# Kernel tuning notes

Hardware: AMD Instinct MI355X
Metric: run time of the kernel (lower is better)

Reference implementation:

```python
import jax, jax.numpy as jnp
import numpy as np

D_MODEL, D_STATE, D_CONV, EXPAND = 1024, 16, 4, 2
D_INNER = EXPAND * D_MODEL            # 2048
DT_RANK = (D_MODEL + 15) // 16        # 64 (mamba 'auto')
B, L = 2, 2048
EPS = 1e-5


def setup_inputs() -> dict:
    key = jax.random.key(0)
    ks = jax.random.split(key, 12)
    s = lambda k, shape, sc=0.02: jax.random.normal(k, shape, dtype=jnp.float32) * sc
    return {
        "x": jax.random.normal(ks[0], (B, L, D_MODEL), dtype=jnp.float32),
        "ln_w": jnp.ones((D_MODEL,), jnp.float32),
        "ln_b": jnp.zeros((D_MODEL,), jnp.float32),
        "W_in": s(ks[1], (2 * D_INNER, D_MODEL)),
        "conv_w": s(ks[2], (D_INNER, D_CONV), 0.2),
        "conv_b": jnp.zeros((D_INNER,), jnp.float32),
        "W_xproj": s(ks[3], (DT_RANK + 2 * D_STATE, D_INNER)),
        "W_dt": s(ks[4], (D_INNER, DT_RANK), 0.1),
        "b_dt": jax.random.uniform(ks[5], (D_INNER,), jnp.float32, -4.0, -2.0),  # softplus(b)~dt_min
        "A_log": jnp.log(jnp.broadcast_to(jnp.arange(1, D_STATE + 1, dtype=jnp.float32), (D_INNER, D_STATE))),
        "D": jnp.ones((D_INNER,), jnp.float32),
        "W_out": s(ks[6], (D_MODEL, D_INNER)),
    }


def _mamba_forward(x, ln_w, ln_b, W_in, conv_w, conv_b, W_xproj, W_dt, b_dt, A_log, D, W_out):
    # Pre-norm LayerNorm
    mu = jnp.mean(x, axis=-1, keepdims=True)
    var = jnp.mean(jnp.square(x - mu), axis=-1, keepdims=True)
    xn = (x - mu) * jax.lax.rsqrt(var + EPS) * ln_w + ln_b

    # in_proj -> [B, L, 2*d_inner]; split into x-branch and gate z
    xz = jnp.einsum("bld,ed->ble", xn, W_in)
    u, z = jnp.split(xz, 2, axis=-1)

    # causal depthwise conv1d over L, kernel width D_CONV
    u_pad = jnp.pad(u, ((0, 0), (D_CONV - 1, 0), (0, 0)))
    uc = conv_b[None, None, :]
    for k in range(D_CONV):
        uc = uc + u_pad[:, k:k + L, :] * conv_w[:, k]
    u = jax.nn.silu(uc)  # [B, L, d_inner]

    # input-dependent dt, B, C
    dbl = jnp.einsum("bld,ed->ble", u, W_xproj)
    dt_r = dbl[..., :DT_RANK]
    Bm = dbl[..., DT_RANK:DT_RANK + D_STATE]          # [B, L, n]
    Cm = dbl[..., DT_RANK + D_STATE:]                 # [B, L, n]
    dt = jax.nn.softplus(jnp.einsum("blr,dr->bld", dt_r, W_dt) + b_dt)  # [B, L, d]

    A = -jnp.exp(A_log)  # [d, n]

    # selective scan over L; carry h: [B, d, n]
    def step(h, inp):
        dt_t, B_t, C_t, u_t = inp  # [B,d], [B,n], [B,n], [B,d]
        dA = jnp.exp(dt_t[:, :, None] * A[None])                 # [B, d, n]
        h = dA * h + (dt_t * u_t)[:, :, None] * B_t[:, None, :]  # [B, d, n]
        y_t = jnp.einsum("bdn,bn->bd", h, C_t)
        return h, y_t

    xs = (jnp.moveaxis(dt, 1, 0), jnp.moveaxis(Bm, 1, 0),
          jnp.moveaxis(Cm, 1, 0), jnp.moveaxis(u, 1, 0))
    h0 = jnp.zeros((x.shape[0], D_INNER, D_STATE), x.dtype)
    _, ys = jax.lax.scan(step, h0, xs)
    y = jnp.moveaxis(ys, 0, 1) + u * D  # [B, L, d_inner]

    y = y * jax.nn.silu(z)
    out = jnp.einsum("bld,ed->ble", y, W_out)
    return x + out


def reference(x, ln_w, ln_b, W_in, conv_w, conv_b, W_xproj, W_dt, b_dt, A_log, D, W_out):
    return _mamba_forward(x, ln_w, ln_b, W_in, conv_w, conv_b, W_xproj, W_dt, b_dt, A_log, D, W_out)
```

## Files before the change

### kernel.cpp

```cpp
#include <hip/hip_runtime.h>
#include <hip/hip_bf16.h>
#include <stdint.h>

typedef __hip_bfloat16 bf16;
typedef __attribute__((ext_vector_type(8))) short short8;
typedef __attribute__((ext_vector_type(4))) short short4v;
typedef __attribute__((ext_vector_type(4))) float floatx4;

#define D_MODEL 1024
#define D_STATE 16
#define D_INNER 2048
#define DT_RANK 64
#define BB 2
#define LL 2048
#define BL (BB * LL)
#define XZ_LD (2 * D_INNER)
#define DBL_LD (DT_RANK + 2 * D_STATE)
#define NCH 64
#define TCH (LL / NCH)

__device__ __forceinline__ bf16 f2b(float f) { return __float2bfloat16(f); }

__device__ __forceinline__ float fsig(float v)  { return __fdividef(1.f, 1.f + __expf(-v)); }
__device__ __forceinline__ float fsoftp(float v){ return fmaxf(v, 0.f) + __logf(1.f + __expf(-fabsf(v))); }

__device__ __forceinline__ void gload16(const void* g, void* l) {
    __builtin_amdgcn_global_load_lds(
        (const __attribute__((address_space(1))) uint32_t*)(uintptr_t)g,
        (__attribute__((address_space(3))) uint32_t*)(uintptr_t)l,
        16, 0, 0);
}

#define S0 (4096 * 1024)
#define S1 (128 * 2048)
#define S2 (2048 * 64)
#define S3 (1024 * 2048)
#define S4 (BL * DBL_LD)
#define WCVT_TOT (S0 + S1 + S2 + S3 + S4)
#define WCVT4 (WCVT_TOT / 4)

__device__ __forceinline__ void cvt4(const float* __restrict__ src,
                                     bf16* __restrict__ dst, int qi) {
    const floatx4 v = *(const floatx4*)(src + (size_t)qi * 4);
    short4v o;
#pragma unroll
    for (int j = 0; j < 4; ++j) {
        bf16 h = f2b(v[j]);
        unsigned short us;
        __builtin_memcpy(&us, &h, 2);
        o[j] = (short)us;
    }
    *(short4v*)(dst + (size_t)qi * 4) = o;
}

__global__ __launch_bounds__(256) void prep_kernel(
    const float* __restrict__ x, const float* __restrict__ w,
    const float* __restrict__ b, bf16* __restrict__ xnb,
    const float* __restrict__ Win, const float* __restrict__ Wx,
    const float* __restrict__ Wdt, const float* __restrict__ Wout,
    bf16* __restrict__ win_bf, bf16* __restrict__ wx_bf,
    bf16* __restrict__ wdt_bf, bf16* __restrict__ wout_bf,
    float* __restrict__ dbl)
{
    __shared__ float s1[256], s2[256];
    const int tid = threadIdx.x;
    if (blockIdx.x < BL) {
        const int row = blockIdx.x;
        const float* xr = x + (size_t)row * D_MODEL;
        float v[4], sum = 0.f, sq = 0.f;
#pragma unroll
        for (int i = 0; i < 4; ++i) {
            v[i] = xr[tid + 256 * i];
            sum += v[i];
            sq  += v[i] * v[i];
        }
        s1[tid] = sum; s2[tid] = sq;
        __syncthreads();
        for (int s = 128; s > 0; s >>= 1) {
            if (tid < s) { s1[tid] += s1[tid + s]; s2[tid] += s2[tid + s]; }
            __syncthreads();
        }
        const float mu  = s1[0] * (1.f / D_MODEL);
        const float var = s2[0] * (1.f / D_MODEL) - mu * mu;
        const float rs  = rsqrtf(var + 1e-5f);
#pragma unroll
        for (int i = 0; i < 4; ++i) {
            const int c = tid + 256 * i;
            xnb[(size_t)row * D_MODEL + c] = f2b((v[i] - mu) * rs * w[c] + b[c]);
        }
    } else {
        int id = (blockIdx.x - BL) * 256 + tid;
        if (id < S0 / 4) { cvt4(Win, win_bf, id); return; }
        id -= S0 / 4;
        if (id < S1 / 4) {
            if (id < (96 * 2048) / 4) cvt4(Wx, wx_bf, id);
            else *(short4v*)(wx_bf + (size_t)id * 4) = (short4v){0, 0, 0, 0};
            return;
        }
        id -= S1 / 4;
        if (id < S2 / 4) { cvt4(Wdt, wdt_bf, id); return; }
        id -= S2 / 4;
        if (id < S3 / 4) { cvt4(Wout, wout_bf, id); return; }
        id -= S3 / 4;
        *(floatx4*)(dbl + (size_t)id * 4) = (floatx4){0.f, 0.f, 0.f, 0.f};
    }
}

#define GTM 128
#define GTN 128
#define GTK 32

template <int EPI>
__global__ __launch_bounds__(256) void gemm_t(
    const bf16* __restrict__ A, int lda,
    const bf16* __restrict__ B, int ldb,
    float* __restrict__ C, int ldc,
    int N, int K,
    const float* __restrict__ bias,
    bf16* __restrict__ C2)
{
    __shared__ short As[GTM * GTK];
    __shared__ short Bs[GTN * GTK];
    const int tid  = threadIdx.x;
    const int lane = tid & 63;
    const int wave = tid >> 6;
    const int wm = (wave & 1) * 64;
    const int wn = (wave >> 1) * 64;
    const int bm = blockIdx.y * GTM;
    const int bn = blockIdx.x * GTN;
    const int kbase = blockIdx.z * K;

    floatx4 acc[4][4];
#pragma unroll
    for (int i = 0; i < 4; ++i)
#pragma unroll
        for (int j = 0; j < 4; ++j) acc[i][j] = (floatx4){0.f, 0.f, 0.f, 0.f};

    const int srow = wave * 16 + (lane >> 2);
    const int scol = (lane & 3) * 8;
    const int fm = lane & 15;
    const int q  = lane >> 4;

    for (int k0 = 0; k0 < K; k0 += GTK) {
#pragma unroll
        for (int r = 0; r < 2; ++r) {
            const int m = r * 64 + srow;
            gload16(A + (size_t)(bm + m) * lda + kbase + k0 + scol,
                    As + m * GTK + scol);
            gload16(B + (size_t)(bn + m) * ldb + kbase + k0 + scol,
                    Bs + m * GTK + scol);
        }
        __syncthreads();

        short8 af[4], bfr[4];
#pragma unroll
        for (int i = 0; i < 4; ++i)
            af[i] = *(short8*)&As[(wm + i * 16 + fm) * GTK + q * 8];
#pragma unroll
        for (int j = 0; j < 4; ++j)
            bfr[j] = *(short8*)&Bs[(wn + j * 16 + fm) * GTK + q * 8];
#pragma unroll
        for (int i = 0; i < 4; ++i)
#pragma unroll
            for (int j = 0; j < 4; ++j)
                acc[i][j] = __builtin_amdgcn_mfma_f32_16x16x32_bf16(
                    af[i], bfr[j], acc[i][j], 0, 0, 0);
        __syncthreads();
    }

    const int col = lane & 15;
    const int rq  = (lane >> 4) * 4;
#pragma unroll
    for (int i = 0; i < 4; ++i) {
#pragma unroll
        for (int j = 0; j < 4; ++j) {
#pragma unroll
            for (int r = 0; r < 4; ++r) {
                const int gm = bm + wm + i * 16 + rq + r;
                const int gn = bn + wn + j * 16 + col;
                if (gn >= N) continue;
                float v = acc[i][j][r];
                if constexpr (EPI == 3) {
                    atomicAdd(&C[(size_t)gm * ldc + gn], v);
                } else if constexpr (EPI == 4) {
                    if (gn < D_INNER) C[(size_t)gm * ldc + gn] = v;
                    else C2[(size_t)gm * (size_t)D_INNER + (gn - D_INNER)] = f2b(v);
                } else {
                    C2[(size_t)gm * ldc + gn] = f2b(fsoftp(v + bias[gn]));
                }
            }
        }
    }
}

#define PNT (D_MODEL / 64)

__global__ __launch_bounds__(512, 2) void gemm256_uz(
    const bf16* __restrict__ A,
    const bf16* __restrict__ B,
    float* __restrict__ U,
    bf16* __restrict__ Z)
{
    __shared__ __attribute__((aligned(16))) short lds[65536];
    const int t    = threadIdx.x;
    const int lane = t & 63;
    const int wid  = t >> 6;
    const int wm   = wid >> 2;
    const int wn   = wid & 3;
    const int fm   = lane & 15;
    const int q    = lane >> 4;

    const int lin = (int)blockIdx.x;
    const int nid = (lin & 7) * 32 + (lin >> 3);
    const int bm  = (nid >> 4) * 256;
    const int bn  = (nid & 15) * 256;

    const int sg   = (((t & 7) ^ ((t >> 3) & 7)) << 3);
    const int ldst = t * 8;
    const short* Agp = (const short*)A + (size_t)(bm + (t >> 3)) * D_MODEL + sg;
    const short* Bgp = (const short*)B + (size_t)(bn + (t >> 3)) * D_MODEL + sg;

#define STG(g, lb) do { \
        gload16((g),                           &lds[(lb) + ldst]);        \
        gload16((g) + (size_t)64 * D_MODEL,    &lds[(lb) + 4096 + ldst]); \
    } while (0)

    const int ss0 = ((q ^ (fm & 7)) << 3);
    const int ss1 = (((4 + q) ^ (fm & 7)) << 3);
    const int aro = fm * 64;
    const int bro = ((wn & 1) * 64 + fm) * 64;

    floatx4 acc[8][4];
#pragma unroll
    for (int i = 0; i < 8; ++i)
#pragma unroll
        for (int j = 0; j < 4; ++j) acc[i][j] = (floatx4){0.f, 0.f, 0.f, 0.f};

    STG(Agp, 0);
    STG(Agp + (size_t)128 * D_MODEL, 8192);
    STG(Bgp, 32768);
    STG(Bgp + (size_t)128 * D_MODEL, 32768 + 8192);

    for (int kt = 0; kt < PNT; ++kt) {
        __syncthreads();
        const int d  = kt & 1;
        const short* Ab = &lds[d * 16384 + wm * 8192];
        const short* Bb = &lds[32768 + d * 16384 + (wn >> 1) * 8192];
        const int kn = (kt + 1) * 64;
        const int nb = (d ^ 1) * 16384;

        short8 bfr[4][2];
#pragma unroll
        for (int cf = 0; cf < 4; ++cf) {
            bfr[cf][0] = *(const short8*)(Bb + bro + cf * 1024 + ss0);
            bfr[cf][1] = *(const short8*)(Bb + bro + cf * 1024 + ss1);
        }

#pragma unroll
        for (int qd = 0; qd < 4; ++qd) {
            short8 af[2][2];
#pragma unroll
            for (int i = 0; i < 2; ++i) {
                af[i][0] = *(const short8*)(Ab + (qd * 2 + i) * 1024 + aro + ss0);
                af[i][1] = *(const short8*)(Ab + (qd * 2 + i) * 1024 + aro + ss1);
            }
            if (qd == 0 && kt < PNT - 1) {
                STG(Agp + kn,                        nb);
                STG(Agp + (size_t)128 * D_MODEL + kn, nb + 8192);
            }
            if (qd == 1 && kt < PNT - 1) {
                STG(Bgp + kn,                        32768 + nb);
                STG(Bgp + (size_t)128 * D_MODEL + kn, 32768 + nb + 8192);
            }
            __builtin_amdgcn_s_barrier();
            __builtin_amdgcn_s_setprio(1);
#pragma unroll
            for (int i = 0; i < 2; ++i)
#pragma unroll
                for (int cf = 0; cf < 4; ++cf) {
                    acc[qd * 2 + i][cf] = __builtin_amdgcn_mfma_f32_16x16x32_bf16(
                        af[i][0], bfr[cf][0], acc[qd * 2 + i][cf], 0, 0, 0);
                    acc[qd * 2 + i][cf] = __builtin_amdgcn_mfma_f32_16x16x32_bf16(
                        af[i][1], bfr[cf][1], acc[qd * 2 + i][cf], 0, 0, 0);
                }
            __builtin_amdgcn_s_setprio(0);
            if (qd < 3) __builtin_amdgcn_s_barrier();
        }
    }
#undef STG

    const int gm0 = bm + wm * 128 + q * 4;
    const int gn0 = bn + wn * 64 + fm;
    if (bn < D_INNER) {
#pragma unroll
        for (int rf = 0; rf < 8; ++rf)
#pragma unroll
            for (int cf = 0; cf < 4; ++cf)
#pragma unroll
                for (int r = 0; r < 4; ++r)
                    U[(size_t)(gm0 + rf * 16 + r) * D_INNER + gn0 + cf * 16] =
                        acc[rf][cf][r];
    } else {
#pragma unroll
        for (int rf = 0; rf < 8; ++rf)
#pragma unroll
            for (int cf = 0; cf < 4; ++cf)
#pragma unroll
                for (int r = 0; r < 4; ++r)
                    Z[(size_t)(gm0 + rf * 16 + r) * D_INNER + gn0 + cf * 16 - D_INNER] =
                        f2b(acc[rf][cf][r]);
    }
}

#define ONT (D_INNER / 64)

__global__ __launch_bounds__(512, 2) void gemm_out8(
    const bf16* __restrict__ A,
    const bf16* __restrict__ B,
    const float* __restrict__ resid,
    float* __restrict__ C)
{
    __shared__ __attribute__((aligned(16))) short lds[32768];
    const int t    = threadIdx.x;
    const int lane = t & 63;
    const int wid  = t >> 6;
    const int wm   = wid >> 2;
    const int wn   = wid & 3;
    const int fm   = lane & 15;
    const int q    = lane >> 4;

    const int lin = (int)blockIdx.x;
    const int nid = (lin & 7) * 32 + (lin >> 3);
    const int bm  = (nid >> 3) * 128;
    const int bn  = (nid & 7) * 128;

    const int sg   = (((t & 7) ^ ((t >> 3) & 7)) << 3);
    const int ldst = t * 8;
    const short* Agp = (const short*)A + (size_t)(bm + (t >> 3)) * D_INNER + sg;
    const short* Bgp = (const short*)B + (size_t)(bn + (t >> 3)) * D_INNER + sg;

#define OSTG(g, lb) do { \
        gload16((g),                        &lds[(lb) + ldst]);        \
        gload16((g) + (size_t)64 * D_INNER, &lds[(lb) + 4096 + ldst]); \
    } while (0)

    const int ss0 = ((q ^ (fm & 7)) << 3);
    const int ss1 = (((4 + q) ^ (fm & 7)) << 3);
    const int fro = fm * 64;

    floatx4 acc[4][2];
#pragma unroll
    for (int i = 0; i < 4; ++i)
#pragma unroll
        for (int j = 0; j < 2; ++j) acc[i][j] = (floatx4){0.f, 0.f, 0.f, 0.f};

    OSTG(Agp, 0);
    OSTG(Bgp, 16384);

    for (int kt = 0; kt < ONT; ++kt) {
        const int d = kt & 1;
        if (kt + 1 < ONT) {
            const int kn = (kt + 1) * 64;
            const int nb = (d ^ 1) * 8192;
            OSTG(Agp + kn, nb);
            OSTG(Bgp + kn, 16384 + nb);
            asm volatile("s_waitcnt vmcnt(4)" ::: "memory");
        } else {
            asm volatile("s_waitcnt vmcnt(0)" ::: "memory");
        }
        __builtin_amdgcn_s_barrier();

        const short* Ab = &lds[d * 8192 + wm * 4096];
        const short* Bb = &lds[16384 + d * 8192 + wn * 2048];

        short8 bfr[2][2];
#pragma unroll
        for (int cf = 0; cf < 2; ++cf) {
            bfr[cf][0] = *(const short8*)(Bb + cf * 1024 + fro + ss0);
            bfr[cf][1] = *(const short8*)(Bb + cf * 1024 + fro + ss1);
        }

#pragma unroll
        for (int qd = 0; qd < 2; ++qd) {
            short8 af[2][2];
#pragma unroll
            for (int i = 0; i < 2; ++i) {
                af[i][0] = *(const short8*)(Ab + (qd * 2 + i) * 1024 + fro + ss0);
                af[i][1] = *(const short8*)(Ab + (qd * 2 + i) * 1024 + fro + ss1);
            }
            __builtin_amdgcn_s_barrier();
            __builtin_amdgcn_s_setprio(1);
#pragma unroll
            for (int i = 0; i < 2; ++i)
#pragma unroll
                for (int cf = 0; cf < 2; ++cf) {
                    acc[qd * 2 + i][cf] = __builtin_amdgcn_mfma_f32_16x16x32_bf16(
                        af[i][0], bfr[cf][0], acc[qd * 2 + i][cf], 0, 0, 0);
                    acc[qd * 2 + i][cf] = __builtin_amdgcn_mfma_f32_16x16x32_bf16(
                        af[i][1], bfr[cf][1], acc[qd * 2 + i][cf], 0, 0, 0);
                }
            __builtin_amdgcn_s_setprio(0);
            __builtin_amdgcn_s_barrier();
        }
    }
#undef OSTG

    const int gm0 = bm + wm * 64 + q * 4;
    const int gn0 = bn + wn * 32 + fm;
#pragma unroll
    for (int i = 0; i < 4; ++i)
#pragma unroll
        for (int cf = 0; cf < 2; ++cf)
#pragma unroll
            for (int r = 0; r < 4; ++r) {
                const size_t idx = (size_t)(gm0 + i * 16 + r) * D_MODEL + gn0 + cf * 16;
                C[idx] = acc[i][cf][r] + resid[idx];
            }
}

#define CCH 128
#define CTC (LL / CCH)

__global__ __launch_bounds__(256) void conv_v2(
    const float* __restrict__ uraw, const float* __restrict__ cw,
    const float* __restrict__ cb, bf16* __restrict__ ucb)
{
    const int blk = blockIdx.x;
    const int c  = blk & (CCH - 1);
    const int dg = (blk >> 7) & 1;
    const int b  = blk >> 8;
    const int d4 = dg * 1024 + threadIdx.x * 4;
    float w0[4], w1[4], w2[4], w3[4], bias[4];
#pragma unroll
    for (int j = 0; j < 4; ++j) {
        bias[j] = cb[d4 + j];
        w0[j] = cw[(d4 + j) * 4 + 0];
        w1[j] = cw[(d4 + j) * 4 + 1];
        w2[j] = cw[(d4 + j) * 4 + 2];
        w3[j] = cw[(d4 + j) * 4 + 3];
    }
    const size_t base = ((size_t)b * LL + (size_t)c * CTC) * D_INNER + d4;
    floatx4 x0 = {0.f, 0.f, 0.f, 0.f}, x1 = x0, x2 = x0;
    if (c > 0) {
        x0 = *(const floatx4*)(uraw + base - 3 * (size_t)D_INNER);
        x1 = *(const floatx4*)(uraw + base - 2 * (size_t)D_INNER);
        x2 = *(const floatx4*)(uraw + base - 1 * (size_t)D_INNER);
    }
#pragma unroll
    for (int tt = 0; tt < CTC; ++tt) {
        const floatx4 x3 = *(const floatx4*)(uraw + base + (size_t)tt * D_INNER);
        short4v o;
#pragma unroll
        for (int j = 0; j < 4; ++j) {
            float a = bias[j] + x0[j] * w0[j] + x1[j] * w1[j]
                              + x2[j] * w2[j] + x3[j] * w3[j];
            a = a * fsig(a);
            bf16 h = f2b(a);
            unsigned short us;
            __builtin_memcpy(&us, &h, 2);
            o[j] = (short)us;
        }
        *(short4v*)(ucb + base + (size_t)tt * D_INNER) = o;
        x0 = x1; x1 = x2; x2 = x3;
    }
}

__global__ __launch_bounds__(256) void cvt_dtr(
    const float* __restrict__ dbl, bf16* __restrict__ dtr_bf)
{
    const int id = blockIdx.x * 256 + threadIdx.x;
    const int m = id >> 6, r = id & 63;
    dtr_bf[id] = f2b(dbl[(size_t)m * DBL_LD + r]);
}

__global__ __launch_bounds__(256) void scan_p1(
    const bf16* __restrict__ uc, const bf16* __restrict__ dtb,
    const float* __restrict__ dbl, const float* __restrict__ A_log,
    float* __restrict__ Psum, float* __restrict__ Hloc)
{
    const int blk = blockIdx.x;
    const int d = (blk & 7) * 256 + threadIdx.x;
    const int c = (blk >> 3) & (NCH - 1);
    const int b = blk >> 9;
    float A[D_STATE], h[D_STATE];
    bool lin = true;
#pragma unroll
    for (int n = 0; n < D_STATE; ++n) {
        A[n] = -__expf(A_log[d * D_STATE + n]);
        lin = lin && (fabsf(A[n] + (float)(n + 1)) < 1e-3f);
        h[n] = 0.f;
    }
    const size_t row0 = (size_t)b * LL + c * TCH;
    const bf16* dtp = dtb + row0 * D_INNER + d;
    const bf16* up  = uc  + row0 * D_INNER + d;
    const float* Bp = dbl + row0 * DBL_LD + DT_RANK;
    float S = 0.f;
    if (lin) {
        for (int t = 0; t < TCH; ++t) {
            const float dtv = (float)dtp[(size_t)t * D_INNER];
            const float uv  = (float)up[(size_t)t * D_INNER];
            const float du  = dtv * uv;
            S += dtv;
            const float e1 = __expf(-dtv);
            float dA = 1.f;
#pragma unroll
            for (int n = 0; n < D_STATE; ++n) {
                dA *= e1;
                h[n] = dA * h[n] + du * Bp[(size_t)t * DBL_LD + n];
            }
        }
    } else {
        for (int t = 0; t < TCH; ++t) {
            const float dtv = (float)dtp[(size_t)t * D_INNER];
            const float uv  = (float)up[(size_t)t * D_INNER];
            const float du  = dtv * uv;
            S += dtv;
#pragma unroll
            for (int n = 0; n < D_STATE; ++n)
                h[n] = __expf(dtv * A[n]) * h[n] + du * Bp[(size_t)t * DBL_LD + n];
        }
    }
    const size_t o = (((size_t)b * NCH + c) * D_INNER + d) * D_STATE;
    if (lin) {
        const float E1 = __expf(-S);
        float P = 1.f;
#pragma unroll
        for (int n = 0; n < D_STATE; ++n) {
            P *= E1;
            Psum[o + n] = P;
            Hloc[o + n] = h[n];
        }
    } else {
#pragma unroll
        for (int n = 0; n < D_STATE; ++n) {
            Psum[o + n] = __expf(S * A[n]);
            Hloc[o + n] = h[n];
        }
    }
}

__global__ __launch_bounds__(256) void scan_p2(
    float* __restrict__ Psum, const float* __restrict__ Hloc)
{
    const int id = blockIdx.x * 256 + threadIdx.x;
    const int dn = id & (D_INNER * D_STATE - 1);
    const int b  = id >> 15;
    float h = 0.f;
    for (int c = 0; c < NCH; ++c) {
        const size_t o = ((size_t)(b * NCH + c) * D_INNER * D_STATE) + dn;
        const float P  = Psum[o];
        const float hl = Hloc[o];
        Psum[o] = h;
        h = P * h + hl;
    }
}

__global__ __launch_bounds__(256) void scan_p3b(
    bf16* __restrict__ ucy, const bf16* __restrict__ dtb,
    const float* __restrict__ dbl, const float* __restrict__ A_log,
    const float* __restrict__ Dw, const float* __restrict__ Hin,
    const bf16* __restrict__ zbf)
{
    const int blk = blockIdx.x;
    const int d = (blk & 7) * 256 + threadIdx.x;
    const int c = (blk >> 3) & (NCH - 1);
    const int b = blk >> 9;
    float A[D_STATE], h[D_STATE];
    const size_t o = (((size_t)b * NCH + c) * D_INNER + d) * D_STATE;
    bool lin = true;
#pragma unroll
    for (int n = 0; n < D_STATE; ++n) {
        A[n] = -__expf(A_log[d * D_STATE + n]);
        lin = lin && (fabsf(A[n] + (float)(n + 1)) < 1e-3f);
        h[n] = Hin[o + n];
    }
    const float Dd = Dw[d];
    const size_t row0 = (size_t)b * LL + c * TCH;
    const bf16* dtp = dtb + row0 * D_INNER + d;
    bf16*       uyp = ucy + row0 * D_INNER + d;
    const float* BCp = dbl + row0 * DBL_LD;
    const bf16* zp   = zbf + row0 * D_INNER + d;
    if (lin) {
        for (int t = 0; t < TCH; ++t) {
            const float dtv = (float)dtp[(size_t)t * D_INNER];
            const float uv  = (float)uyp[(size_t)t * D_INNER];
            const float du  = dtv * uv;
            float acc = uv * Dd;
            const float* Brow = BCp + (size_t)t * DBL_LD + DT_RANK;
            const float* Crow = Brow + D_STATE;
            const float e1 = __expf(-dtv);
            float dA = 1.f;
#pragma unroll
            for (int n = 0; n < D_STATE; ++n) {
                dA *= e1;
                h[n] = dA * h[n] + du * Brow[n];
                acc += h[n] * Crow[n];
            }
            const float zv = (float)zp[(size_t)t * D_INNER];
            uyp[(size_t)t * D_INNER] = f2b(acc * zv * fsig(zv));
        }
    } else {
        for (int t = 0; t < TCH; ++t) {
            const float dtv = (float)dtp[(size_t)t * D_INNER];
            const float uv  = (float)uyp[(size_t)t * D_INNER];
            const float du  = dtv * uv;
            float acc = uv * Dd;
            const float* Brow = BCp + (size_t)t * DBL_LD + DT_RANK;
            const float* Crow = Brow + D_STATE;
#pragma unroll
            for (int n = 0; n < D_STATE; ++n) {
                h[n] = __expf(dtv * A[n]) * h[n] + du * Brow[n];
                acc += h[n] * Crow[n];
            }
            const float zv = (float)zp[(size_t)t * D_INNER];
            uyp[(size_t)t * D_INNER] = f2b(acc * zv * fsig(zv));
        }
    }
}

#define BM 128
#define BN 128
#define BK 8

__global__ __launch_bounds__(256) void ln_kernel(
    const float* __restrict__ x, const float* __restrict__ w,
    const float* __restrict__ b, float* __restrict__ xnf)
{
    __shared__ float s1[256], s2[256];
    const int row = blockIdx.x;
    const int tid = threadIdx.x;
    const float* xr = x + (size_t)row * D_MODEL;
    float v[4], sum = 0.f, sq = 0.f;
#pragma unroll
    for (int i = 0; i < 4; ++i) {
        v[i] = xr[tid + 256 * i];
        sum += v[i];
        sq  += v[i] * v[i];
    }
    s1[tid] = sum; s2[tid] = sq;
    __syncthreads();
    for (int s = 128; s > 0; s >>= 1) {
        if (tid < s) { s1[tid] += s1[tid + s]; s2[tid] += s2[tid + s]; }
        __syncthreads();
    }
    const float mu  = s1[0] * (1.f / D_MODEL);
    const float var = s2[0] * (1.f / D_MODEL) - mu * mu;
    const float rs  = rsqrtf(var + 1e-5f);
#pragma unroll
    for (int i = 0; i < 4; ++i) {
        const int c = tid + 256 * i;
        xnf[(size_t)row * D_MODEL + c] = (v[i] - mu) * rs * w[c] + b[c];
    }
}

__global__ __launch_bounds__(256) void gemm_bt(
    const float* __restrict__ A, int lda,
    const float* __restrict__ Bw,
    float* __restrict__ C, int ldc,
    int M, int N, int K, int epi,
    const float* __restrict__ bias,
    const float* __restrict__ resid)
{
    __shared__ float As[BK][BM + 1];
    __shared__ float Bs[BK][BN + 1];
    const int tx = threadIdx.x, ty = threadIdx.y;
    const int tid = ty * 16 + tx;
    const int bm = blockIdx.y * BM, bn = blockIdx.x * BN;
    float acc[8][8];
#pragma unroll
    for (int i = 0; i < 8; ++i)
#pragma unroll
        for (int j = 0; j < 8; ++j) acc[i][j] = 0.f;
    for (int k0 = 0; k0 < K; k0 += BK) {
#pragma unroll
        for (int i = tid; i < BM * BK; i += 256) {
            const int m = i / BK, kk = i % BK;
            As[kk][m] = A[(size_t)(bm + m) * lda + (k0 + kk)];
        }
#pragma unroll
        for (int i = tid; i < BN * BK; i += 256) {
            const int n = i / BK, kk = i % BK;
            const int gn = bn + n;
            Bs[kk][n] = (gn < N) ? Bw[(size_t)gn * K + (k0 + kk)] : 0.f;
        }
        __syncthreads();
#pragma unroll
        for (int kk = 0; kk < BK; ++kk) {
            float av[8], bv[8];
#pragma unroll
            for (int i = 0; i < 8; ++i) av[i] = As[kk][ty * 8 + i];
#pragma unroll
            for (int j = 0; j < 8; ++j) bv[j] = Bs[kk][tx * 8 + j];
#pragma unroll
            for (int i = 0; i < 8; ++i)
#pragma unroll
                for (int j = 0; j < 8; ++j) acc[i][j] += av[i] * bv[j];
        }
        __syncthreads();
    }
#pragma unroll
    for (int i = 0; i < 8; ++i) {
        const int gm = bm + ty * 8 + i;
#pragma unroll
        for (int j = 0; j < 8; ++j) {
            const int gn = bn + tx * 8 + j;
            if (gn >= N) continue;
            float v = acc[i][j];
            if (epi == 1) {
                v += bias[gn];
                v = fmaxf(v, 0.f) + log1pf(expf(-fabsf(v)));
            } else if (epi == 2) {
                v += resid[(size_t)gm * ldc + gn];
            }
            C[(size_t)gm * ldc + gn] = v;
        }
    }
}

__global__ __launch_bounds__(256) void conv_silu_kernel(
    float* __restrict__ xz, const float* __restrict__ cw,
    const float* __restrict__ cb)
{
    const int idx = blockIdx.x * 256 + threadIdx.x;
    const int b = idx >> 11, d = idx & (D_INNER - 1);
    const float w0 = cw[d * 4 + 0], w1 = cw[d * 4 + 1];
    const float w2 = cw[d * 4 + 2], w3 = cw[d * 4 + 3];
    const float bias = cb[d];
    float* u = xz + (size_t)b * LL * XZ_LD + d;
    float x0 = 0.f, x1 = 0.f, x2 = 0.f;
    for (int t = 0; t < LL; ++t) {
        const float x3 = u[(size_t)t * XZ_LD];
        const float c = bias + x0 * w0 + x1 * w1 + x2 * w2 + x3 * w3;
        u[(size_t)t * XZ_LD] = c / (1.f + expf(-c));
        x0 = x1; x1 = x2; x2 = x3;
    }
}

__global__ __launch_bounds__(256) void scan_kernel(
    float* __restrict__ xz, const float* __restrict__ dtb,
    const float* __restrict__ dbl,
    const float* __restrict__ A_log, const float* __restrict__ Dw)
{
    const int idx = blockIdx.x * 256 + threadIdx.x;
    const int b = idx >> 11, d = idx & (D_INNER - 1);
    float A[D_STATE], h[D_STATE];
#pragma unroll
    for (int n = 0; n < D_STATE; ++n) {
        A[n] = -expf(A_log[d * D_STATE + n]);
        h[n] = 0.f;
    }
    const float Dd = Dw[d];
    const float* dtp  = dtb + (size_t)b * LL * D_INNER + d;
    float*       up   = xz  + (size_t)b * LL * XZ_LD + d;
    const float* dblp = dbl + (size_t)b * LL * DBL_LD;
    for (int t = 0; t < LL; ++t) {
        const float dtv = dtp[(size_t)t * D_INNER];
        const float uv  = up[(size_t)t * XZ_LD];
        const float zv  = up[(size_t)t * XZ_LD + D_INNER];
        const float* Brow = dblp + (size_t)t * DBL_LD + DT_RANK;
        const float* Crow = Brow + D_STATE;
        const float du = dtv * uv;
        float acc = uv * Dd;
#pragma unroll
        for (int n = 0; n < D_STATE; ++n) {
            const float dA = expf(dtv * A[n]);
            h[n] = dA * h[n] + du * Brow[n];
            acc += h[n] * Crow[n];
        }
        const float sz = zv / (1.f + expf(-zv));
        up[(size_t)t * XZ_LD] = acc * sz;
    }
}

extern "C" void kernel_launch(void* const* d_in, const int* in_sizes, int n_in,
                              void* d_out, int out_size, void* d_ws, size_t ws_size,
                              hipStream_t stream)
{
    const float* x       = (const float*)d_in[0];
    const float* ln_w    = (const float*)d_in[1];
    const float* ln_b    = (const float*)d_in[2];
    const float* W_in    = (const float*)d_in[3];
    const float* conv_w  = (const float*)d_in[4];
    const float* conv_b  = (const float*)d_in[5];
    const float* W_xproj = (const float*)d_in[6];
    const float* W_dt    = (const float*)d_in[7];
    const float* b_dt    = (const float*)d_in[8];
    const float* A_log   = (const float*)d_in[9];
    const float* Dw      = (const float*)d_in[10];
    const float* W_out   = (const float*)d_in[11];
    float* out = (float*)d_out;

    float* wsf     = (float*)d_ws;
    bf16*  dtb_bf  = (bf16*)wsf;
    float* uraw    = wsf + 4194304;
    bf16*  zbf     = (bf16*)(wsf + 12582912);
    float* Psum    = wsf + 16777216;
    float* Hloc    = wsf + 20971520;
    float* dbl     = wsf + 25165824;
    bf16*  ucy     = (bf16*)(wsf + 25559040);
    bf16*  xn_bf   = (bf16*)(wsf + 29753344);
    bf16*  win_bf  = (bf16*)(wsf + 31850496);
    bf16*  wx_bf   = (bf16*)(wsf + 33947648);
    bf16*  wdt_bf  = (bf16*)(wsf + 34078720);
    bf16*  wout_bf = (bf16*)(wsf + 34144256);
    bf16*  dtr_bf  = (bf16*)(wsf + 35192832);
    const size_t need_big = (size_t)35323904 * sizeof(float);

    if (ws_size >= need_big) {
        prep_kernel<<<BL + WCVT4 / 256, 256, 0, stream>>>(
            x, ln_w, ln_b, xn_bf,
            W_in, W_xproj, W_dt, W_out, win_bf, wx_bf, wdt_bf, wout_bf, dbl);
        gemm256_uz<<<dim3(256), 512, 0, stream>>>(xn_bf, win_bf, uraw, zbf);
        conv_v2<<<BB * 2 * CCH, 256, 0, stream>>>(uraw, conv_w, conv_b, ucy);
        gemm_t<3><<<dim3(1, BL / GTM, 8), 256, 0, stream>>>(
            ucy, D_INNER, wx_bf, D_INNER, dbl, DBL_LD,
            DBL_LD, D_INNER / 8, nullptr, nullptr);
        cvt_dtr<<<BL * DT_RANK / 256, 256, 0, stream>>>(dbl, dtr_bf);
        gemm_t<5><<<dim3(D_INNER / GTN, BL / GTM, 1), 256, 0, stream>>>(
            dtr_bf, DT_RANK, wdt_bf, DT_RANK, nullptr, D_INNER,
            D_INNER, DT_RANK, b_dt, dtb_bf);
        scan_p1<<<BB * NCH * 8, 256, 0, stream>>>(
            ucy, dtb_bf, dbl, A_log, Psum, Hloc);
        scan_p2<<<BB * D_INNER * D_STATE / 256, 256, 0, stream>>>(Psum, Hloc);
        scan_p3b<<<BB * NCH * 8, 256, 0, stream>>>(
            ucy, dtb_bf, dbl, A_log, Dw, Psum, zbf);
        gemm_out8<<<dim3(256), 512, 0, stream>>>(ucy, wout_bf, x, out);
    } else {
        float* fdtb = wsf;
        float* fxn  = fdtb;
        float* fxz  = fdtb + (size_t)BL * D_INNER;
        float* fdbl = fxz + (size_t)BL * XZ_LD;
        ln_kernel<<<BL, 256, 0, stream>>>(x, ln_w, ln_b, fxn);
        dim3 blk(16, 16);
        gemm_bt<<<dim3(XZ_LD / BN, BL / BM), blk, 0, stream>>>(
            fxn, D_MODEL, W_in, fxz, XZ_LD, BL, XZ_LD, D_MODEL, 0, nullptr, nullptr);
        conv_silu_kernel<<<(BB * D_INNER) / 256, 256, 0, stream>>>(fxz, conv_w, conv_b);
        gemm_bt<<<dim3(1, BL / BM), blk, 0, stream>>>(
            fxz, XZ_LD, W_xproj, fdbl, DBL_LD, BL, DBL_LD, D_INNER, 0, nullptr, nullptr);
        gemm_bt<<<dim3(D_INNER / BN, BL / BM), blk, 0, stream>>>(
            fdbl, DBL_LD, W_dt, fdtb, D_INNER, BL, D_INNER, DT_RANK, 1, b_dt, nullptr);
        scan_kernel<<<(BB * D_INNER) / 256, 256, 0, stream>>>(fxz, fdtb, fdbl, A_log, Dw);
        gemm_bt<<<dim3(D_MODEL / BN, BL / BM), blk, 0, stream>>>(
            fxz, XZ_LD, W_out, out, D_MODEL, BL, D_MODEL, D_INNER, 2, nullptr, x);
    }
}
```

Measured before the change: 279.1 us.

## Replace in_proj GEMM with 256x128 tile, BK=32 kernel for higher occupancy

Rewrites the in_proj GEMM from a 256x256 tile with BK=64 and 128KB LDS to a 256x128 tile with BK=32 and 48KB LDS, launching 512 blocks instead of 256. The new loop uses explicit vmcnt waits and a simpler double-buffered prefetch, and launch bounds allow 4 blocks per CU. The intent is more occupancy and better CU coverage with less LDS per block. The cost is lower arithmetic intensity per block, more global traffic for B reuse, and more barriers per unit of work.

```diff
diff --git a/kernel.cpp b/kernel.cpp
--- a/kernel.cpp
+++ b/kernel.cpp
@@ -193,107 +193,86 @@
     }
 }
 
-#define PNT (D_MODEL / 64)
-
-__global__ __launch_bounds__(512, 2) void gemm256_uz(
+#define UNT (D_MODEL / 32)
+
+__global__ __launch_bounds__(512, 4) void gemm_uz2(
     const bf16* __restrict__ A,
     const bf16* __restrict__ B,
     float* __restrict__ U,
     bf16* __restrict__ Z)
 {
-    __shared__ __attribute__((aligned(16))) short lds[65536];
+    __shared__ __attribute__((aligned(16))) short lds[24576];
     const int t    = threadIdx.x;
     const int lane = t & 63;
     const int wid  = t >> 6;
-    const int wm   = wid >> 2;
-    const int wn   = wid & 3;
+    const int wm   = wid >> 1;
+    const int wn   = wid & 1;
     const int fm   = lane & 15;
     const int q    = lane >> 4;
 
     const int lin = (int)blockIdx.x;
-    const int nid = (lin & 7) * 32 + (lin >> 3);
-    const int bm  = (nid >> 4) * 256;
-    const int bn  = (nid & 15) * 256;
-
-    const int sg   = (((t & 7) ^ ((t >> 3) & 7)) << 3);
-    const int ldst = t * 8;
-    const short* Agp = (const short*)A + (size_t)(bm + (t >> 3)) * D_MODEL + sg;
-    const short* Bgp = (const short*)B + (size_t)(bn + (t >> 3)) * D_MODEL + sg;
-
-#define STG(g, lb) do { \
-        gload16((g),                           &lds[(lb) + ldst]);        \
-        gload16((g) + (size_t)64 * D_MODEL,    &lds[(lb) + 4096 + ldst]); \
+    const int nid = (lin & 7) * 64 + (lin >> 3);
+    const int bm  = (nid >> 5) * 256;
+    const int bn  = (nid & 31) * 128;
+
+    const int sg = (((t & 3) ^ ((t >> 2) & 3)) << 3);
+    const short* Agp = (const short*)A + (size_t)(bm + (t >> 2)) * D_MODEL + sg;
+    const short* Bgp = (const short*)B + (size_t)(bn + (t >> 2)) * D_MODEL + sg;
+
+#define USTG(koff, d) do { \
+        gload16(Agp + (koff),                        &lds[(d) * 8192 + t * 8]);        \
+        gload16(Agp + (size_t)128 * D_MODEL + (koff), &lds[(d) * 8192 + 4096 + t * 8]); \
+        gload16(Bgp + (koff),                        &lds[16384 + (d) * 4096 + t * 8]); \
     } while (0)
 
-    const int ss0 = ((q ^ (fm & 7)) << 3);
-    const int ss1 = (((4 + q) ^ (fm & 7)) << 3);
-    const int aro = fm * 64;
-    const int bro = ((wn & 1) * 64 + fm) * 64;
-
-    floatx4 acc[8][4];
-#pragma unroll
-    for (int i = 0; i < 8; ++i)
+    const int ss = ((q ^ (fm & 3)) << 3);
+
+    floatx4 acc[4][4];
+#pragma unroll
+    for (int i = 0; i < 4; ++i)
 #pragma unroll
         for (int j = 0; j < 4; ++j) acc[i][j] = (floatx4){0.f, 0.f, 0.f, 0.f};
 
-    STG(Agp, 0);
-    STG(Agp + (size_t)128 * D_MODEL, 8192);
-    STG(Bgp, 32768);
-    STG(Bgp + (size_t)128 * D_MODEL, 32768 + 8192);
-
-    for (int kt = 0; kt < PNT; ++kt) {
-        __syncthreads();
-        const int d  = kt & 1;
-        const short* Ab = &lds[d * 16384 + wm * 8192];
-        const short* Bb = &lds[32768 + d * 16384 + (wn >> 1) * 8192];
-        const int kn = (kt + 1) * 64;
-        const int nb = (d ^ 1) * 16384;
-
-        short8 bfr[4][2];
-#pragma unroll
-        for (int cf = 0; cf < 4; ++cf) {
-            bfr[cf][0] = *(const short8*)(Bb + bro + cf * 1024 + ss0);
-            bfr[cf][1] = *(const short8*)(Bb + bro + cf * 1024 + ss1);
-        }
-
-#pragma unroll
-        for (int qd = 0; qd < 4; ++qd) {
-            short8 af[2][2];
-#pragma unroll
-            for (int i = 0; i < 2; ++i) {
-                af[i][0] = *(const short8*)(Ab + (qd * 2 + i) * 1024 + aro + ss0);
-                af[i][1] = *(const short8*)(Ab + (qd * 2 + i) * 1024 + aro + ss1);
-            }
-            if (qd == 0 && kt < PNT - 1) {
-                STG(Agp + kn,                        nb);
-                STG(Agp + (size_t)128 * D_MODEL + kn, nb + 8192);
-            }
-            if (qd == 1 && kt < PNT - 1) {
-                STG(Bgp + kn,                        32768 + nb);
-                STG(Bgp + (size_t)128 * D_MODEL + kn, 32768 + nb + 8192);
-            }
-            __builtin_amdgcn_s_barrier();
-            __builtin_amdgcn_s_setprio(1);
-#pragma unroll
-            for (int i = 0; i < 2; ++i)
-#pragma unroll
-                for (int cf = 0; cf < 4; ++cf) {
-                    acc[qd * 2 + i][cf] = __builtin_amdgcn_mfma_f32_16x16x32_bf16(
-                        af[i][0], bfr[cf][0], acc[qd * 2 + i][cf], 0, 0, 0);
-                    acc[qd * 2 + i][cf] = __builtin_amdgcn_mfma_f32_16x16x32_bf16(
-                        af[i][1], bfr[cf][1], acc[qd * 2 + i][cf], 0, 0, 0);
-                }
-            __builtin_amdgcn_s_setprio(0);
-            if (qd < 3) __builtin_amdgcn_s_barrier();
-        }
-    }
-#undef STG
-
-    const int gm0 = bm + wm * 128 + q * 4;
+    USTG(0, 0);
+
+    for (int kt = 0; kt < UNT; ++kt) {
+        const int d = kt & 1;
+        if (kt + 1 < UNT) {
+            USTG((kt + 1) * 32, d ^ 1);
+            asm volatile("s_waitcnt vmcnt(3)" ::: "memory");
+        } else {
+            asm volatile("s_waitcnt vmcnt(0)" ::: "memory");
+        }
+        __builtin_amdgcn_s_barrier();
+
+        const short* Ab = &lds[d * 8192 + wm * 2048];
+        const short* Bb = &lds[16384 + d * 4096 + wn * 2048];
+
+        short8 af[4], bfr[4];
+#pragma unroll
+        for (int rf = 0; rf < 4; ++rf)
+            af[rf] = *(const short8*)(Ab + (rf * 16 + fm) * 32 + ss);
+#pragma unroll
+        for (int cf = 0; cf < 4; ++cf)
+            bfr[cf] = *(const short8*)(Bb + (cf * 16 + fm) * 32 + ss);
+
+        __builtin_amdgcn_s_setprio(1);
+#pragma unroll
+        for (int rf = 0; rf < 4; ++rf)
+#pragma unroll
+            for (int cf = 0; cf < 4; ++cf)
+                acc[rf][cf] = __builtin_amdgcn_mfma_f32_16x16x32_bf16(
+                    af[rf], bfr[cf], acc[rf][cf], 0, 0, 0);
+        __builtin_amdgcn_s_setprio(0);
+        __builtin_amdgcn_s_barrier();
+    }
+#undef USTG
+
+    const int gm0 = bm + wm * 64 + q * 4;
     const int gn0 = bn + wn * 64 + fm;
     if (bn < D_INNER) {
 #pragma unroll
-        for (int rf = 0; rf < 8; ++rf)
+        for (int rf = 0; rf < 4; ++rf)
 #pragma unroll
             for (int cf = 0; cf < 4; ++cf)
 #pragma unroll
@@ -302,7 +281,7 @@
                         acc[rf][cf][r];
     } else {
 #pragma unroll
-        for (int rf = 0; rf < 8; ++rf)
+        for (int rf = 0; rf < 4; ++rf)
 #pragma unroll
             for (int cf = 0; cf < 4; ++cf)
 #pragma unroll
@@ -810,7 +789,7 @@
         prep_kernel<<<BL + WCVT4 / 256, 256, 0, stream>>>(
             x, ln_w, ln_b, xn_bf,
             W_in, W_xproj, W_dt, W_out, win_bf, wx_bf, wdt_bf, wout_bf, dbl);
-        gemm256_uz<<<dim3(256), 512, 0, stream>>>(xn_bf, win_bf, uraw, zbf);
+        gemm_uz2<<<dim3(512), 512, 0, stream>>>(xn_bf, win_bf, uraw, zbf);
         conv_v2<<<BB * 2 * CCH, 256, 0, stream>>>(uraw, conv_w, conv_b, ucy);
         gemm_t<3><<<dim3(1, BL / GTM, 8), 256, 0, stream>>>(
             ucy, D_INNER, wx_bf, D_INNER, dbl, DBL_LD,
```

Measured after the change: 284.4 us. Within noise of the previous version (+1.9%).
